# Kernel tuning notes

Measured on AMD Instinct MI355X. Metric: run time of the kernel, lower is better.

The kernel has to match this reference:

```python
import jax, jax.numpy as jnp
import numpy as np

NUM_CLASSES = 81
IOU_THR = 0.5
NEG_POS_RATIO = 3


def _cxcywh_to_xyxy(b):
    cx, cy, w, h = b[..., 0], b[..., 1], b[..., 2], b[..., 3]
    return jnp.stack([cx - w / 2, cy - h / 2, cx + w / 2, cy + h / 2], axis=-1)


def _xyxy_to_cxcywh(b):
    x1, y1, x2, y2 = b[..., 0], b[..., 1], b[..., 2], b[..., 3]
    return jnp.stack([(x1 + x2) / 2, (y1 + y2) / 2, x2 - x1, y2 - y1], axis=-1)


def _iou(b1, b2):
    # b1 (M,4), b2 (A,4) in xyxy -> (M,A) pairwise IoU
    lt = jnp.maximum(b1[:, None, :2], b2[None, :, :2])
    rb = jnp.minimum(b1[:, None, 2:], b2[None, :, 2:])
    wh = jnp.clip(rb - lt, 0.0)
    inter = wh[..., 0] * wh[..., 1]
    a1 = (b1[:, 2] - b1[:, 0]) * (b1[:, 3] - b1[:, 1])
    a2 = (b2[:, 2] - b2[:, 0]) * (b2[:, 3] - b2[:, 1])
    union = a1[:, None] + a2[None, :] - inter
    return inter / (union + 1e-7)


def _match_one(gt_boxes, gt_labels, anchors_xyxy, anchors_cxcywh):
    # gt_boxes (M,4) xyxy, gt_labels (M,) -> per-anchor targets
    M = gt_boxes.shape[0]
    iou = _iou(gt_boxes, anchors_xyxy)          # (M, A)
    gt_best_iou = iou.max(axis=1)               # best anchor per GT
    gt_best_idx = iou.argmax(axis=1)
    a_best_iou = iou.max(axis=0)                # best GT per anchor
    a_best_idx = iou.argmax(axis=0)
    pos = a_best_iou > IOU_THR

    # sequential force-assignment (faithful to the torch per-object loop)
    def body(j, carry):
        pos, a_idx = carry
        ba = gt_best_idx[j]
        valid = gt_best_iou[j] > 1e-5
        pos = pos.at[ba].set(jnp.where(valid, True, pos[ba]))
        override = valid & (a_best_iou[ba] < gt_best_iou[j])
        a_idx = a_idx.at[ba].set(jnp.where(override, j, a_idx[ba]))
        return pos, a_idx

    pos, a_idx = jax.lax.fori_loop(0, M, body, (pos, a_best_idx))
    mb = _xyxy_to_cxcywh(gt_boxes[a_idx])       # (A,4) matched GT in cxcywh
    acx = anchors_cxcywh
    enc = jnp.stack([
        (mb[:, 0] - acx[:, 0]) / acx[:, 2],
        (mb[:, 1] - acx[:, 1]) / acx[:, 3],
        jnp.log(mb[:, 2] / acx[:, 2] + 1e-7),
        jnp.log(mb[:, 3] / acx[:, 3] + 1e-7)], axis=-1)
    true_locs = jnp.where(pos[:, None], enc, 0.0)
    true_cls = jnp.where(pos, gt_labels[a_idx] + 1, 0)
    return true_locs, true_cls, pos


def setup_inputs() -> dict:
    key = jax.random.key(0)
    kb, kl, kcx, kwh, kax, kaw, ks = jax.random.split(key, 7)
    B, A, M, C = 32, 24564, 20, NUM_CLASSES
    cxy = 0.2 + 0.6 * jax.random.uniform(kcx, (B, M, 2))
    wh = 0.05 + 0.25 * jax.random.uniform(kwh, (B, M, 2))
    gt_boxes = jnp.concatenate([cxy - wh / 2, cxy + wh / 2], axis=-1)  # valid xyxy
    gt_labels = jax.random.randint(kl, (B, M), 0, C - 1)
    acxy = jax.random.uniform(kax, (A, 2))
    awh = 0.04 + 0.3 * jax.random.uniform(kaw, (A, 2))
    anchors_cxcywh = jnp.concatenate([acxy, awh], axis=-1)
    predicted_locs = jax.random.normal(kb, (B, A, 4), jnp.float32)
    predicted_scores = jax.random.normal(ks, (B, A, C), jnp.float32)
    return {"predicted_locs": predicted_locs, "predicted_scores": predicted_scores,
            "gt_boxes": gt_boxes, "gt_labels": gt_labels,
            "anchors_cxcywh": anchors_cxcywh}


def reference(predicted_locs, predicted_scores, gt_boxes, gt_labels, anchors_cxcywh):
    B, A, C = predicted_scores.shape
    anchors_xyxy = _cxcywh_to_xyxy(anchors_cxcywh)
    true_locs, true_cls, pos = jax.vmap(_match_one, in_axes=(0, 0, None, None))(
        gt_boxes, gt_labels, anchors_xyxy, anchors_cxcywh)
    # SmoothL1 (beta=1, reduction='sum') over positive anchors only
    d = jnp.abs(predicted_locs - true_locs)
    sl1 = jnp.where(d < 1.0, 0.5 * d * d, d - 0.5)
    loc_loss = jnp.sum(sl1 * pos[..., None])
    # per-anchor cross entropy
    logp = jax.nn.log_softmax(predicted_scores, axis=-1)
    conf_all = -jnp.take_along_axis(logp, true_cls[..., None], axis=-1)[..., 0]  # (B,A)
    # hard negative mining
    n_pos = pos.sum(axis=1)                                   # (B,)
    n_keep = jnp.where(n_pos > 0,
                       jnp.minimum(NEG_POS_RATIO * n_pos, A - n_pos),
                       jnp.minimum(NEG_POS_RATIO * 20, A))
    neg_scores = jnp.where(pos, -jnp.inf, conf_all)           # positives never selected
    order = jnp.argsort(-neg_scores, axis=1)                  # descending
    ranks = jnp.argsort(order, axis=1)                        # 0 == hardest negative
    hard_neg = (ranks < n_keep[:, None]) & ~pos
    final_mask = pos | hard_neg
    conf_loss = jnp.sum(conf_all * final_mask)
    n_pos_total = jnp.maximum(n_pos.sum(), 1).astype(jnp.float32)
    total = (loc_loss + conf_loss) / n_pos_total
    return total, loc_loss / n_pos_total, conf_loss / n_pos_total
```

## Files before the change

kernel.cpp:

```cpp
#include <hip/hip_runtime.h>
#include <float.h>
#include <stdint.h>

#define NEG_POS_RATIO 3
#define MAXM 64
#define CHUNK 1024

__device__ __forceinline__ float smooth_l1(float d) {
    float a = fabsf(d);
    return a < 1.0f ? 0.5f * a * a : a - 0.5f;
}
__device__ __forceinline__ unsigned key_of(float f) {
    unsigned u = __float_as_uint(f);
    return (u & 0x80000000u) ? ~u : (u | 0x80000000u);
}
__device__ __forceinline__ float val_of(unsigned k) {
    return __uint_as_float((k & 0x80000000u) ? (k ^ 0x80000000u) : ~k);
}

__global__ void __launch_bounds__(256) k_init(
    unsigned long long* __restrict__ gbest, float* __restrict__ loc_loss,
    float* __restrict__ pos_conf, int* __restrict__ n_pos, int BM, int B)
{
    const int t = blockIdx.x * blockDim.x + threadIdx.x;
    if (t < BM) gbest[t] = 0ULL;
    if (t < B) { loc_loss[t] = 0.0f; pos_conf[t] = 0.0f; n_pos[t] = 0; }
}

__global__ void __launch_bounds__(256) k_gtbest(
    const float*  __restrict__ gt_boxes,
    const float4* __restrict__ anchors,
    int A, int M,
    unsigned long long* __restrict__ gbest)
{
    const int b = blockIdx.y, tid = threadIdx.x;
    const int base = blockIdx.x * CHUNK;
    __shared__ float              s_gt[MAXM * 4];
    __shared__ unsigned long long s_best[MAXM];
    if (tid < M * 4) s_gt[tid] = gt_boxes[(size_t)b * M * 4 + tid];
    if (tid < M) s_best[tid] = 0ULL;
    __syncthreads();

    float ax1[4], ay1[4], ax2[4], ay2[4], aarea[4];
    bool  val[4];
#pragma unroll
    for (int i = 0; i < 4; ++i) {
        const int a = base + tid + i * 256;
        val[i] = a < A;
        if (val[i]) {
            const float4 an = anchors[a];
            const float hx = an.z * 0.5f, hy = an.w * 0.5f;
            ax1[i] = an.x - hx; ay1[i] = an.y - hy;
            ax2[i] = an.x + hx; ay2[i] = an.y + hy;
            aarea[i] = an.z * an.w;
        } else { ax1[i]=ay1[i]=ax2[i]=ay2[i]=aarea[i]=0.0f; }
    }
    for (int j = 0; j < M; ++j) {
        const float gx1 = s_gt[4*j+0], gy1 = s_gt[4*j+1];
        const float gx2 = s_gt[4*j+2], gy2 = s_gt[4*j+3];
        const float garea = (gx2 - gx1) * (gy2 - gy1);
        unsigned long long best = 0ULL;
#pragma unroll
        for (int i = 0; i < 4; ++i) {
            if (!val[i]) continue;
            const float w = fmaxf(fminf(gx2, ax2[i]) - fmaxf(gx1, ax1[i]), 0.0f);
            const float h = fmaxf(fminf(gy2, ay2[i]) - fmaxf(gy1, ay1[i]), 0.0f);
            const float inter = w * h;
            const float iou = inter / ((garea + aarea[i] - inter) + 1e-7f);
            const unsigned a_idx = (unsigned)(base + tid + i * 256);
            const unsigned long long pk =
                ((unsigned long long)__float_as_uint(iou) << 32)
              | (unsigned long long)(0xFFFFFFFFu - a_idx);
            if (pk > best) best = pk;
        }
#pragma unroll
        for (int off = 32; off; off >>= 1) {
            const unsigned long long o = __shfl_xor(best, off);
            if (o > best) best = o;
        }
        if ((tid & 63) == 0) atomicMax(&s_best[j], best);
    }
    __syncthreads();
    if (tid < M) atomicMax(&gbest[(size_t)b * M + tid], s_best[tid]);
}

__global__ void __launch_bounds__(256) k_assign(
    const float4* __restrict__ pred_locs,
    const float*  __restrict__ gt_boxes,
    const int*    __restrict__ gt_labels,
    const float4* __restrict__ anchors,
    int A, int M,
    const unsigned long long* __restrict__ gbest,
    float* __restrict__ loc_loss, int* __restrict__ n_pos,
    int* __restrict__ cls_out)
{
    const int b = blockIdx.y, tid = threadIdx.x;
    const int base = blockIdx.x * CHUNK;
    __shared__ float s_gt[MAXM * 4];
    __shared__ int   s_lab[MAXM];
    __shared__ float s_gbi[MAXM];
    __shared__ int   s_gbx[MAXM];
    if (tid < M * 4) s_gt[tid] = gt_boxes[(size_t)b * M * 4 + tid];
    if (tid < M) {
        s_lab[tid] = gt_labels[(size_t)b * M + tid];
        const unsigned long long v = gbest[(size_t)b * M + tid];
        s_gbi[tid] = __uint_as_float((unsigned)(v >> 32));
        s_gbx[tid] = (int)(0xFFFFFFFFu - (unsigned)(v & 0xFFFFFFFFull));
    }
    __syncthreads();

    float lsum = 0.0f;
    int   np   = 0;
#pragma unroll
    for (int i = 0; i < 4; ++i) {
        const int a = base + tid + i * 256;
        if (a >= A) continue;
        const float4 an = anchors[a];
        const float hx = an.z * 0.5f, hy = an.w * 0.5f;
        const float ax1 = an.x - hx, ay1 = an.y - hy;
        const float ax2 = an.x + hx, ay2 = an.y + hy;
        const float aarea = an.z * an.w;
        float abest = -1.0f; int aidx = 0;
        for (int j = 0; j < M; ++j) {
            const float gx1 = s_gt[4*j+0], gy1 = s_gt[4*j+1];
            const float gx2 = s_gt[4*j+2], gy2 = s_gt[4*j+3];
            const float garea = (gx2 - gx1) * (gy2 - gy1);
            const float w = fmaxf(fminf(gx2, ax2) - fmaxf(gx1, ax1), 0.0f);
            const float h = fmaxf(fminf(gy2, ay2) - fmaxf(gy1, ay1), 0.0f);
            const float inter = w * h;
            const float iou = inter / ((garea + aarea - inter) + 1e-7f);
            if (iou > abest) { abest = iou; aidx = j; }
        }
        bool pos = abest > 0.5f;
        int midx = aidx;
        for (int j = 0; j < M; ++j) {
            if (s_gbx[j] == a && s_gbi[j] > 1e-5f) {
                pos = true;
                if (abest < s_gbi[j]) midx = j;
            }
        }
        int cls = 0;
        if (pos) {
            const float gx1 = s_gt[4*midx+0], gy1 = s_gt[4*midx+1];
            const float gx2 = s_gt[4*midx+2], gy2 = s_gt[4*midx+3];
            const float mcx = (gx1 + gx2) * 0.5f, mcy = (gy1 + gy2) * 0.5f;
            const float mw = gx2 - gx1, mh = gy2 - gy1;
            const float e0 = (mcx - an.x) / an.z;
            const float e1 = (mcy - an.y) / an.w;
            const float e2 = logf(mw / an.z + 1e-7f);
            const float e3 = logf(mh / an.w + 1e-7f);
            const float4 p = pred_locs[(size_t)b * A + a];
            lsum += smooth_l1(p.x - e0) + smooth_l1(p.y - e1)
                  + smooth_l1(p.z - e2) + smooth_l1(p.w - e3);
            ++np;
            cls = s_lab[midx] + 1;
        }
        cls_out[(size_t)b * A + a] = cls;
    }
#pragma unroll
    for (int off = 32; off; off >>= 1) {
        lsum += __shfl_xor(lsum, off);
        np   += __shfl_xor(np, off);
    }
    if ((tid & 63) == 0) {
        atomicAdd(&loc_loss[b], lsum);
        atomicAdd(&n_pos[b], np);
    }
}

__global__ void __launch_bounds__(256) k_conf81v2(
    const float* __restrict__ scores,
    const int*   __restrict__ cls_arr,
    float* __restrict__ pos_conf,
    unsigned* __restrict__ keys,
    int A, int total)
{
    __shared__ float lds[64 * 81];
    const int tid   = threadIdx.x;
    const int first = blockIdx.x * 64;

    const float4* src4 = (const float4*)scores + (size_t)blockIdx.x * 1296;
    float4 v[5];
#pragma unroll
    for (int k = 0; k < 5; ++k) v[k] = src4[tid + k * 256];
    float4 vt = make_float4(0.f, 0.f, 0.f, 0.f);
    if (tid < 16) vt = src4[1280 + tid];

    const int row_l = tid >> 2;
    const int sub4  = tid & 3;
    const int c = cls_arr[first + row_l];

    float4* lds4 = (float4*)lds;
#pragma unroll
    for (int k = 0; k < 5; ++k) lds4[tid + k * 256] = v[k];
    if (tid < 16) lds4[1280 + tid] = vt;
    __syncthreads();

    const float* rp = lds + row_l * 81;
    float s = 0.0f, t = -FLT_MAX;
#pragma unroll
    for (int k = 0; k < 20; ++k) {
        const int idx = sub4 + 4 * k;
        const float val = rp[idx];
        s += __expf(val);
        t = (idx == c) ? val : t;
    }
    if (sub4 == 0) {
        const float val = rp[80];
        s += __expf(val);
        t = (c == 80) ? val : t;
    }
    s += __shfl_xor(s, 1);  t = fmaxf(t, __shfl_xor(t, 1));
    s += __shfl_xor(s, 2);  t = fmaxf(t, __shfl_xor(t, 2));

    if (sub4 == 0) {
        const int row = first + row_l;
        const float conf = __logf(s) - t;
        if (c > 0) {
            atomicAdd(&pos_conf[row / A], conf);
            keys[row] = 0u;
        } else {
            keys[row] = key_of(conf);
        }
    }
}

__global__ void __launch_bounds__(256) k_conf81(
    const float* __restrict__ scores,
    const int*   __restrict__ cls_arr,
    float* __restrict__ pos_conf,
    unsigned* __restrict__ keys,
    int A, int total)
{
    const int tid  = threadIdx.x;
    const int wav  = tid >> 6;
    const int lane = tid & 63;
    const int sub  = lane & 15;
    const int row  = (blockIdx.x * 4 + wav) * 4 + (lane >> 4);
    if (row >= total) return;

    const float* rp = scores + (size_t)row * 81;
    const int c = cls_arr[row];
    const float v0 = rp[sub];
    const float v1 = rp[sub + 16];
    const float v2 = rp[sub + 32];
    const float v3 = rp[sub + 48];
    const float v4 = rp[sub + 64];
    float v5 = 0.0f;
    const bool has5 = (sub == 0);
    if (has5) v5 = rp[80];

    float s = __expf(v0) + __expf(v1) + __expf(v2) + __expf(v3) + __expf(v4);
    if (has5) s += __expf(v5);
    float t = -FLT_MAX;
    t = (sub      == c) ? v0 : t;
    t = (sub + 16 == c) ? v1 : t;
    t = (sub + 32 == c) ? v2 : t;
    t = (sub + 48 == c) ? v3 : t;
    t = (sub + 64 == c) ? v4 : t;
    if (has5 && c == 80) t = v5;
#pragma unroll
    for (int off = 8; off; off >>= 1) {
        s += __shfl_xor(s, off);
        t  = fmaxf(t, __shfl_xor(t, off));
    }
    if (sub == 0) {
        const float conf = __logf(s) - t;
        if (c > 0) {
            atomicAdd(&pos_conf[row / A], conf);
            keys[row] = 0u;
        } else {
            keys[row] = key_of(conf);
        }
    }
}

__global__ void __launch_bounds__(256) k_conf_gen(
    const float* __restrict__ scores, const int* __restrict__ cls_arr,
    float* __restrict__ pos_conf, unsigned* __restrict__ keys,
    int A, int C, int total)
{
    const int tid  = threadIdx.x;
    const int lane = tid & 63;
    const int sub  = lane & 15;
    const int row  = (blockIdx.x * 4 + (tid >> 6)) * 4 + (lane >> 4);
    float s = 0.0f, sc = -FLT_MAX;
    int cls = 0;
    const bool active = row < total;
    if (active) {
        cls = cls_arr[row];
        const float* rpp = scores + (size_t)row * C;
        for (int idx = sub; idx < C; idx += 16) {
            const float v = rpp[idx];
            s += __expf(v);
            if (idx == cls) sc = v;
        }
    }
#pragma unroll
    for (int off = 8; off; off >>= 1) {
        s  += __shfl_xor(s, off);
        sc  = fmaxf(sc, __shfl_xor(sc, off));
    }
    if (active && sub == 0) {
        const float conf = __logf(s) - sc;
        if (cls > 0) { atomicAdd(&pos_conf[row / A], conf); keys[row] = 0u; }
        else keys[row] = key_of(conf);
    }
}

__device__ __forceinline__ void hist_add(
    int* hist, unsigned key, unsigned pref, int shift, bool first, int lane,
    bool valid)
{
    const bool ok = valid &&
        (first || ((key >> (shift + 8)) == (pref >> (shift + 8))));
    if (ok) {
        const int bin = (key >> shift) & 255;
        unsigned long long mm = __ballot(1);
#pragma unroll
        for (int bit = 0; bit < 8; ++bit) {
            const unsigned long long bb = __ballot((bin >> bit) & 1);
            mm &= ((bin >> bit) & 1) ? bb : ~bb;
        }
        if ((mm & ((1ULL << lane) - 1)) == 0)
            atomicAdd(&hist[bin], (int)__popcll(mm));
    }
}

__global__ void __launch_bounds__(1024) k_select(
    const unsigned* __restrict__ keys, const int* __restrict__ n_pos,
    float* __restrict__ neg_conf, int A, int M)
{
    const int b    = blockIdx.x;
    const int tid  = threadIdx.x;
    const int lane = tid & 63;
    const unsigned* kb = keys + (size_t)b * A;
    const int np = n_pos[b];
    const int k = (np > 0) ? min(NEG_POS_RATIO * np, A - np)
                           : min(NEG_POS_RATIO * M, A);
    __shared__ int      hist[256];
    __shared__ unsigned s_pref;
    __shared__ int      s_rem;
    if (k <= 0) { if (tid == 0) neg_conf[b] = 0.0f; return; }
    if (tid == 0) { s_pref = 0u; s_rem = k; }

    const int A4   = A >> 2;
    const int tail = A - (A4 << 2);
    const uint4* kb4 = (const uint4*)kb;
    __syncthreads();

    for (int pass = 0; pass < 4; ++pass) {
        const int shift = 24 - 8 * pass;
        if (tid < 256) hist[tid] = 0;
        __syncthreads();
        const unsigned pref = s_pref;
        const bool first = (pass == 0);
        for (int base = 0; base < A4; base += 8 * 1024) {
            uint4 kk[8]; bool ok[8];
#pragma unroll
            for (int u = 0; u < 8; ++u) {
                const int i = base + tid + u * 1024;
                ok[u] = (i < A4);
                kk[u] = ok[u] ? kb4[i] : uint4{0, 0, 0, 0};
            }
#pragma unroll
            for (int u = 0; u < 8; ++u) {
                hist_add(hist, kk[u].x, pref, shift, first, lane, ok[u]);
                hist_add(hist, kk[u].y, pref, shift, first, lane, ok[u]);
                hist_add(hist, kk[u].z, pref, shift, first, lane, ok[u]);
                hist_add(hist, kk[u].w, pref, shift, first, lane, ok[u]);
            }
        }
        if (tid < tail) hist_add(hist, kb[(A4 << 2) + tid], pref, shift, first,
                                 lane, true);
        __syncthreads();
        if (tid == 0) {
            int rem = s_rem, cum = 0, bsel = 0;
            for (int i = 255; i >= 0; --i) {
                const int c = hist[i];
                if (cum + c >= rem) { bsel = i; s_rem = rem - cum; break; }
                cum += c;
            }
            s_pref = pref | ((unsigned)bsel << shift);
        }
        __syncthreads();
    }
    const unsigned kth = s_pref;
    float sum = 0.0f; int cnt = 0;
    for (int base = 0; base < A4; base += 8 * 1024) {
        uint4 kk[8]; bool ok[8];
#pragma unroll
        for (int u = 0; u < 8; ++u) {
            const int i = base + tid + u * 1024;
            ok[u] = (i < A4);
            kk[u] = ok[u] ? kb4[i] : uint4{0, 0, 0, 0};
        }
#pragma unroll
        for (int u = 0; u < 8; ++u) {
            if (kk[u].x > kth) { sum += val_of(kk[u].x); ++cnt; }
            if (kk[u].y > kth) { sum += val_of(kk[u].y); ++cnt; }
            if (kk[u].z > kth) { sum += val_of(kk[u].z); ++cnt; }
            if (kk[u].w > kth) { sum += val_of(kk[u].w); ++cnt; }
        }
    }
    if (tid < tail) {
        const unsigned key = kb[(A4 << 2) + tid];
        if (key > kth) { sum += val_of(key); ++cnt; }
    }
#pragma unroll
    for (int off = 32; off; off >>= 1) {
        sum += __shfl_xor(sum, off);
        cnt += __shfl_xor(cnt, off);
    }
    __shared__ float s_sum[16];
    __shared__ int   s_cnt[16];
    const int w = tid >> 6;
    if (lane == 0) { s_sum[w] = sum; s_cnt[w] = cnt; }
    __syncthreads();
    if (tid == 0) {
        float ts = 0.0f; int tc = 0;
        const int nw = (int)(blockDim.x >> 6);
        for (int i = 0; i < nw; ++i) { ts += s_sum[i]; tc += s_cnt[i]; }
        neg_conf[b] = ts + (float)(k - tc) * val_of(kth);
    }
}

__global__ void __launch_bounds__(64) k_final(
    const float* __restrict__ loc_loss,
    const float* __restrict__ pos_conf,
    const float* __restrict__ neg_conf,
    const int*   __restrict__ n_pos,
    int B, float* __restrict__ out)
{
    const int tid = threadIdx.x;
    float L = 0.0f, Cs = 0.0f;
    int   np = 0;
    for (int b = tid; b < B; b += 64) {
        L  += loc_loss[b];
        Cs += pos_conf[b] + neg_conf[b];
        np += n_pos[b];
    }
#pragma unroll
    for (int off = 32; off; off >>= 1) {
        L  += __shfl_xor(L, off);
        Cs += __shfl_xor(Cs, off);
        np += __shfl_xor(np, off);
    }
    if (tid == 0) {
        const float denom = (float)(np > 1 ? np : 1);
        out[0] = (L + Cs) / denom;
        out[1] = L / denom;
        out[2] = Cs / denom;
    }
}

extern "C" void kernel_launch(void* const* d_in, const int* in_sizes, int n_in,
                              void* d_out, int out_size, void* d_ws, size_t ws_size,
                              hipStream_t stream) {
    const float* pred_locs = (const float*)d_in[0];
    const float* scores    = (const float*)d_in[1];
    const float* gt_boxes  = (const float*)d_in[2];
    const int*   gt_labels = (const int*)d_in[3];
    const float* anchors   = (const float*)d_in[4];

    const int A = in_sizes[4] / 4;
    const int B = (int)((long long)in_sizes[0] / (4LL * A));
    const int M = in_sizes[3] / B;
    const int C = (int)((long long)in_sizes[1] / ((long long)B * A));
    float* out = (float*)d_out;

    char* ws = (char*)d_ws;
    float* loc_loss = (float*)ws;
    float* pos_conf = loc_loss + B;
    float* neg_conf = pos_conf + B;
    int*   n_pos    = (int*)(neg_conf + B);
    size_t off = (size_t)(((16LL * B) + 255) / 256) * 256;
    unsigned long long* gbest = (unsigned long long*)(ws + off);
    off += (size_t)(((8LL * B * M) + 255) / 256) * 256;
    int*      cls_arr = (int*)(ws + off);
    unsigned* keys    = (unsigned*)(ws + off + (size_t)B * A * sizeof(int));

    const int NCHUNK = (A + CHUNK - 1) / CHUNK;

    k_init<<<(B * M + 255) / 256, 256, 0, stream>>>(gbest, loc_loss, pos_conf, n_pos,
                                                    B * M, B);
    k_gtbest<<<dim3(NCHUNK, B), 256, 0, stream>>>(gt_boxes, (const float4*)anchors,
                                                  A, M, gbest);
    k_assign<<<dim3(NCHUNK, B), 256, 0, stream>>>((const float4*)pred_locs, gt_boxes,
                                                  gt_labels, (const float4*)anchors,
                                                  A, M, gbest, loc_loss, n_pos, cls_arr);

    const int total = (int)((long long)B * A);
    if (C == 81 && (total & 63) == 0) {
        k_conf81v2<<<dim3((unsigned)(total / 64)), 256, 0, stream>>>(
            scores, cls_arr, pos_conf, keys, A, total);
    } else if (C == 81) {
        const int nblk = (total + 15) / 16;
        k_conf81<<<dim3((unsigned)nblk), 256, 0, stream>>>(scores, cls_arr, pos_conf,
                                                           keys, A, total);
    } else {
        const int nblk = (total + 15) / 16;
        k_conf_gen<<<dim3((unsigned)nblk), 256, 0, stream>>>(scores, cls_arr, pos_conf,
                                                             keys, A, C, total);
    }

    k_select<<<B, 1024, 0, stream>>>(keys, n_pos, neg_conf, A, M);

    k_final<<<1, 64, 0, stream>>>(loc_loss, pos_conf, neg_conf, n_pos, B, out);
}
```

Measured before the change: 713.7 us.

## Make 81-class conf kernel persistent with register-prefetch of next tile

The per-anchor cross-entropy kernel becomes a grid-stride persistent kernel capped at 2048 blocks. While the current tile is computed from LDS, each block prefetches the next tile's scores into registers, overlapping global loads with exp/log compute. This trades higher register use and an extra barrier per tile for fewer block launches and latency hiding.

Result: faster. 664.7 us (-6.9%).

```diff
diff --git a/kernel.cpp b/kernel.cpp
--- a/kernel.cpp
+++ b/kernel.cpp
@@ -168,59 +168,72 @@
     }
 }
 
-__global__ void __launch_bounds__(256) k_conf81v2(
+__global__ void __launch_bounds__(256) k_conf81v3(
     const float* __restrict__ scores,
     const int*   __restrict__ cls_arr,
     float* __restrict__ pos_conf,
     unsigned* __restrict__ keys,
-    int A, int total)
+    int A, int ntile)
 {
     __shared__ float lds[64 * 81];
-    const int tid   = threadIdx.x;
-    const int first = blockIdx.x * 64;
-
-    const float4* src4 = (const float4*)scores + (size_t)blockIdx.x * 1296;
+    const int tid    = threadIdx.x;
+    const int row_l  = tid >> 2;
+    const int sub4   = tid & 3;
+    const int stride = gridDim.x;
+
+    int tile = blockIdx.x;
     float4 v[5];
-#pragma unroll
-    for (int k = 0; k < 5; ++k) v[k] = src4[tid + k * 256];
     float4 vt = make_float4(0.f, 0.f, 0.f, 0.f);
-    if (tid < 16) vt = src4[1280 + tid];
-
-    const int row_l = tid >> 2;
-    const int sub4  = tid & 3;
-    const int c = cls_arr[first + row_l];
-
+    {
+        const float4* src4 = (const float4*)scores + (size_t)tile * 1296;
+#pragma unroll
+        for (int k = 0; k < 5; ++k) v[k] = src4[tid + k * 256];
+        if (tid < 16) vt = src4[1280 + tid];
+    }
     float4* lds4 = (float4*)lds;
-#pragma unroll
-    for (int k = 0; k < 5; ++k) lds4[tid + k * 256] = v[k];
-    if (tid < 16) lds4[1280 + tid] = vt;
-    __syncthreads();
-
-    const float* rp = lds + row_l * 81;
-    float s = 0.0f, t = -FLT_MAX;
-#pragma unroll
-    for (int k = 0; k < 20; ++k) {
-        const int idx = sub4 + 4 * k;
-        const float val = rp[idx];
-        s += __expf(val);
-        t = (idx == c) ? val : t;
-    }
-    if (sub4 == 0) {
-        const float val = rp[80];
-        s += __expf(val);
-        t = (c == 80) ? val : t;
-    }
-    s += __shfl_xor(s, 1);  t = fmaxf(t, __shfl_xor(t, 1));
-    s += __shfl_xor(s, 2);  t = fmaxf(t, __shfl_xor(t, 2));
-
-    if (sub4 == 0) {
-        const int row = first + row_l;
-        const float conf = __logf(s) - t;
-        if (c > 0) {
-            atomicAdd(&pos_conf[row / A], conf);
-            keys[row] = 0u;
-        } else {
-            keys[row] = key_of(conf);
+
+    for (; tile < ntile; tile += stride) {
+        __syncthreads();
+#pragma unroll
+        for (int k = 0; k < 5; ++k) lds4[tid + k * 256] = v[k];
+        if (tid < 16) lds4[1280 + tid] = vt;
+        const int c = cls_arr[tile * 64 + row_l];
+        __syncthreads();
+
+        const int nxt = tile + stride;
+        if (nxt < ntile) {
+            const float4* src4 = (const float4*)scores + (size_t)nxt * 1296;
+#pragma unroll
+            for (int k = 0; k < 5; ++k) v[k] = src4[tid + k * 256];
+            if (tid < 16) vt = src4[1280 + tid];
+        }
+
+        const float* rp = lds + row_l * 81;
+        float s = 0.0f, t = -FLT_MAX;
+#pragma unroll
+        for (int k = 0; k < 20; ++k) {
+            const int idx = sub4 + 4 * k;
+            const float val = rp[idx];
+            s += __expf(val);
+            t = (idx == c) ? val : t;
+        }
+        if (sub4 == 0) {
+            const float val = rp[80];
+            s += __expf(val);
+            t = (c == 80) ? val : t;
+        }
+        s += __shfl_xor(s, 1);  t = fmaxf(t, __shfl_xor(t, 1));
+        s += __shfl_xor(s, 2);  t = fmaxf(t, __shfl_xor(t, 2));
+
+        if (sub4 == 0) {
+            const int row = tile * 64 + row_l;
+            const float conf = __logf(s) - t;
+            if (c > 0) {
+                atomicAdd(&pos_conf[row / A], conf);
+                keys[row] = 0u;
+            } else {
+                keys[row] = key_of(conf);
+            }
         }
     }
 }
@@ -492,8 +505,10 @@
 
     const int total = (int)((long long)B * A);
     if (C == 81 && (total & 63) == 0) {
-        k_conf81v2<<<dim3((unsigned)(total / 64)), 256, 0, stream>>>(
-            scores, cls_arr, pos_conf, keys, A, total);
+        const int ntile = total / 64;
+        const int grid  = ntile < 2048 ? ntile : 2048;
+        k_conf81v3<<<dim3((unsigned)grid), 256, 0, stream>>>(
+            scores, cls_arr, pos_conf, keys, A, ntile);
     } else if (C == 81) {
         const int nblk = (total + 15) / 16;
         k_conf81<<<dim3((unsigned)nblk), 256, 0, stream>>>(scores, cls_arr, pos_conf,
```
